# Performance work log

Measured on AMD Instinct MI355X. Metric: run time of the kernel, lower is better.

Reference implementation:

```python
import jax, jax.numpy as jnp
import numpy as np

N, F, H, C = 8192, 512, 512, 64
SPARSITY = 0.5  # args.linear_sparsity


def _percentile(t, q):
    # torch kthvalue semantics: k = 1 + round(0.01*q*(n-1)), 1-indexed k-th smallest
    n = t.size
    k = int(1 + round(0.01 * q * (n - 1)))
    return jnp.sort(t.ravel())[k - 1]


def _pair_norm(x):
    x = x - x.mean(axis=0)
    rownorm_mean = jnp.sqrt(1e-6 + (x * x).sum(axis=1).mean())
    return x / rownorm_mean


def setup_inputs() -> dict:
    key = jax.random.key(0)
    ks = jax.random.split(key, 8)
    x = jax.random.normal(ks[0], (N, F), jnp.float32)
    adj = (jax.random.uniform(ks[1], (N, N)) < 0.002).astype(jnp.float32)
    W0 = jax.random.normal(ks[2], (H, F), jnp.float32) * (1.0 / np.sqrt(F))
    W1 = jax.random.normal(ks[3], (H, H), jnp.float32) * (1.0 / np.sqrt(H))
    W2 = jax.random.normal(ks[4], (C, H), jnp.float32) * (1.0 / np.sqrt(H))
    S0 = jax.random.normal(ks[5], (H, F), jnp.float32)
    S1 = jax.random.normal(ks[6], (H, H), jnp.float32)
    S2 = jax.random.normal(ks[7], (C, H), jnp.float32)
    return {"x": x, "adj": adj, "W0": W0, "W1": W1, "W2": W2,
            "S0": S0, "S1": S1, "S2": S2}


def reference(x, adj, W0, W1, W2, S0, S1, S2):
    # add self loops
    idx = jnp.arange(N)
    adj = adj.at[idx, idx].set(1.0)
    # global threshold over all |score| params (enable_abs_comp=True)
    all_scores = jnp.concatenate([jnp.abs(S0).ravel(), jnp.abs(S1).ravel(), jnp.abs(S2).ravel()])
    thr = _percentile(all_scores, SPARSITY * 100.0)
    # symmetric normalization D^-1/2 A D^-1/2
    deg_inv_sqrt = jnp.maximum(adj.sum(axis=-1), 1.0) ** -0.5
    adj_n = deg_inv_sqrt[:, None] * adj * deg_inv_sqrt[None, :]

    def masked_linear(h, W, S):
        Wm = W * (jnp.abs(S) > thr).astype(W.dtype)
        return h @ Wm.T

    # layers 0..num_layers-2 applied back-to-back (as in the source loop)
    h = masked_linear(x, W0, S0)
    h = masked_linear(h, W1, S1)
    h = adj_n @ h            # aggregation: [N,N] @ [N,H]
    h = _pair_norm(h)
    h = jax.nn.relu(h)
    h = masked_linear(h, W2, S2)
    return adj_n @ h          # [N, C]
```

## Files before the change

kernel.cpp:

```cpp
#include <hip/hip_runtime.h>
#include <hip/hip_bf16.h>

#define NN 8192
#define FF 512
#define HH 512
#define CC 64
#define NS_TOTAL 557056
#define KSEL 278529u
#define MAXNBR 96
#define MASKB 2176

typedef short short8 __attribute__((ext_vector_type(8)));
typedef __bf16 bf16x8 __attribute__((ext_vector_type(8)));
typedef float f32x4 __attribute__((ext_vector_type(4)));

__device__ inline unsigned short f2bf(float f) {
    unsigned u = __float_as_uint(f);
    u += 0x7fffu + ((u >> 16) & 1u);
    return (unsigned short)(u >> 16);
}
__device__ inline float bf2f(unsigned short h) {
    return __uint_as_float(((unsigned)h) << 16);
}

__device__ inline f32x4 mfma16x16x32(short8 a, short8 b, f32x4 c) {
    return __builtin_amdgcn_mfma_f32_16x16x32_bf16(
        __builtin_bit_cast(bf16x8, a), __builtin_bit_cast(bf16x8, b), c, 0, 0, 0);
}

__device__ inline void gload_lds16(const unsigned short* g, unsigned short* l) {
    __builtin_amdgcn_global_load_lds(
        (const __attribute__((address_space(1))) void*)g,
        (__attribute__((address_space(3))) void*)l,
        16, 0, 0);
}

__device__ void deg_row_body(const float* __restrict__ adj, int* __restrict__ nnz,
                             int* __restrict__ colsI, float* __restrict__ dis,
                             int row, int* dcnt) {
    const int t = threadIdx.x;
    if (t == 0) *dcnt = 0;
    __syncthreads();
    const float4* arow = (const float4*)(adj + (size_t)row * NN);
    int* cp = colsI + (size_t)row * MAXNBR;
    for (int c4 = t; c4 < NN / 4; c4 += 256) {
        float4 v = arow[c4];
        int base = c4 * 4;
        float vv[4] = {v.x, v.y, v.z, v.w};
#pragma unroll
        for (int kq = 0; kq < 4; ++kq) {
            int col = base + kq;
            if (vv[kq] != 0.f || col == row) {
                int s = atomicAdd(dcnt, 1);
                if (s < MAXNBR) cp[s] = col;
            }
        }
    }
    __syncthreads();
    if (t == 0) {
        int c = *dcnt;
        nnz[row] = (c < MAXNBR) ? c : MAXNBR;
        dis[row] = rsqrtf((float)c);
    }
}

__device__ void isel(const unsigned* __restrict__ hist, unsigned k,
                     unsigned& bin, unsigned& krem) {
    __shared__ unsigned sh[256];
    __shared__ unsigned res[2];
    const int t = threadIdx.x;
    __syncthreads();
    sh[t] = hist[t];
    __syncthreads();
    unsigned pre = 0;
    for (int i = 0; i < t; ++i) pre += sh[i];
    if (pre < k && k <= pre + sh[t]) { res[0] = (unsigned)t; res[1] = k - pre; }
    __syncthreads();
    bin = res[0]; krem = res[1];
}

__device__ void isel_chain(const unsigned* __restrict__ hists, int npass,
                           unsigned& prefix, unsigned& k) {
    prefix = 0; k = KSEL;
    for (int p = 0; p < npass; ++p) {
        unsigned bin, krem;
        isel(hists + p * 256, k, bin, krem);
        prefix |= bin << (24 - 8 * p);
        k = krem;
    }
}


__global__ __launch_bounds__(256) void hist8_kernel(const float* __restrict__ S0,
                                                    const float* __restrict__ S1,
                                                    const float* __restrict__ S2,
                                                    unsigned* __restrict__ hists, int pass,
                                                    const float* __restrict__ adj,
                                                    int* __restrict__ nnz, int* __restrict__ colsI,
                                                    float* __restrict__ dis, int degRow0) {
    __shared__ unsigned lh[256];
    __shared__ int dcnt;
    if ((int)blockIdx.x >= 256) {
        deg_row_body(adj, nnz, colsI, dis, degRow0 + (int)blockIdx.x - 256, &dcnt);
        return;
    }
    unsigned prefix = 0, k;
    if (pass > 0) isel_chain(hists, pass, prefix, k);
    unsigned pmask = (pass > 0) ? (0xFFFFFFFFu << (32 - 8 * pass)) : 0u;
    int shift = 24 - 8 * pass;
    __syncthreads();
    lh[threadIdx.x] = 0;
    __syncthreads();
    for (int idx = blockIdx.x * 256 + threadIdx.x; idx < NS_TOTAL; idx += 65536) {
        float v = (idx < 262144) ? S0[idx] : (idx < 524288) ? S1[idx - 262144] : S2[idx - 524288];
        unsigned key = __float_as_uint(fabsf(v));
        if ((key & pmask) == prefix)
            atomicAdd(&lh[(key >> shift) & 0xffu], 1u);
    }
    __syncthreads();
    unsigned c = lh[threadIdx.x];
    if (c) atomicAdd(&hists[pass * 256 + threadIdx.x], c);
}


__global__ __launch_bounds__(256) void mask_split_fused(
        const float* __restrict__ W0, const float* __restrict__ W1,
        const float* __restrict__ W2, const float* __restrict__ S0,
        const float* __restrict__ S1, const float* __restrict__ S2,
        const unsigned* __restrict__ hists,
        unsigned short* __restrict__ W0h, unsigned short* __restrict__ W0l,
        unsigned short* __restrict__ W1h, unsigned short* __restrict__ W1l,
        unsigned short* __restrict__ W2h, unsigned short* __restrict__ W2l,
        const float* __restrict__ X,
        unsigned short* __restrict__ Xh, unsigned short* __restrict__ Xl) {
    if (blockIdx.x >= MASKB) {
        int i = (blockIdx.x - MASKB) * 256 + threadIdx.x;
        float4 v = ((const float4*)X)[i];
        float vv[4] = {v.x, v.y, v.z, v.w};
        ushort4 hi, lo;
        unsigned short* hp = (unsigned short*)&hi;
        unsigned short* lp = (unsigned short*)&lo;
#pragma unroll
        for (int j = 0; j < 4; ++j) {
            hp[j] = f2bf(vv[j]);
            lp[j] = f2bf(vv[j] - bf2f(hp[j]));
        }
        *(ushort4*)&Xh[(size_t)i * 4] = hi;
        *(ushort4*)&Xl[(size_t)i * 4] = lo;
        return;
    }
    unsigned prefix, k;
    isel_chain(hists, 4, prefix, k);
    float thr = __uint_as_float(prefix);
    int idx = blockIdx.x * 256 + threadIdx.x;
    const float* W; const float* S; unsigned short* Yh; unsigned short* Yl; int i;
    if (idx < 262144)      { W = W0; S = S0; Yh = W0h; Yl = W0l; i = idx; }
    else if (idx < 524288) { W = W1; S = S1; Yh = W1h; Yl = W1l; i = idx - 262144; }
    else                   { W = W2; S = S2; Yh = W2h; Yl = W2l; i = idx - 524288; }
    float v = (fabsf(S[i]) > thr) ? W[i] : 0.f;
    unsigned short hi = f2bf(v);
    Yh[i] = hi;
    Yl[i] = f2bf(v - bf2f(hi));
}


template<int BMt, int BNt, int WRITE_SPLIT>
__global__ __launch_bounds__(256) void gemm_hl(
        const unsigned short* __restrict__ Ah, const unsigned short* __restrict__ Al,
        const unsigned short* __restrict__ Bh, const unsigned short* __restrict__ Bl,
        float* __restrict__ Cf, unsigned short* __restrict__ Ch,
        unsigned short* __restrict__ Cl, int Nn, int gridN, int gemmBlocks,
        const float* __restrict__ adj, int* __restrict__ nnz, int* __restrict__ colsI,
        float* __restrict__ dis, int degRow0) {
    constexpr int BK = 32;
    constexpr int MF = BMt / 32, NF = BNt / 32;
    __shared__ __align__(16) unsigned short AhS[BMt * BK], AlS[BMt * BK];
    __shared__ __align__(16) unsigned short BhS[BNt * BK], BlS[BNt * BK];
    __shared__ int dcnt;

    if ((int)blockIdx.x >= gemmBlocks) {
        deg_row_body(adj, nnz, colsI, dis, degRow0 + (int)blockIdx.x - gemmBlocks, &dcnt);
        return;
    }
    const int tid = threadIdx.x, lane = tid & 63, wid = tid >> 6;
    const int wr = wid >> 1, wc = wid & 1;
    const int bm = ((int)blockIdx.x / gridN) * BMt;
    const int bn = ((int)blockIdx.x % gridN) * BNt;
    const int r16 = lane & 15, kg = lane >> 4;
    const int srow = lane >> 2;
    const int scol = ((lane & 3) ^ ((srow >> 1) & 3)) * 8;
    constexpr int cA = BMt / 16, cB = BNt / 16, CPW = (2 * cA + 2 * cB) / 4;
    f32x4 acc[MF][NF] = {};

    const int ksw = (kg ^ ((r16 >> 1) & 3)) * 8;
    const unsigned short* pAh = &AhS[(wr * (BMt / 2) + r16) * BK + ksw];
    const unsigned short* pAl = &AlS[(wr * (BMt / 2) + r16) * BK + ksw];
    const unsigned short* pBh = &BhS[(wc * (BNt / 2) + r16) * BK + ksw];
    const unsigned short* pBl = &BlS[(wc * (BNt / 2) + r16) * BK + ksw];

    for (int k0 = 0; k0 < 512; k0 += BK) {
        __syncthreads();
#pragma unroll
        for (int i = 0; i < CPW; ++i) {
            int c = wid * CPW + i;
            const unsigned short* src; unsigned short* dst; int cc, r0;
            if (c < cA)               { src = Ah; dst = AhS; cc = c;               r0 = bm + cc * 16; }
            else if (c < 2 * cA)      { src = Al; dst = AlS; cc = c - cA;          r0 = bm + cc * 16; }
            else if (c < 2 * cA + cB) { src = Bh; dst = BhS; cc = c - 2 * cA;      r0 = bn + cc * 16; }
            else                      { src = Bl; dst = BlS; cc = c - 2 * cA - cB; r0 = bn + cc * 16; }
            gload_lds16(src + (size_t)(r0 + srow) * 512 + k0 + scol, dst + cc * 512);
        }
        __syncthreads();
        short8 bhf[NF], blf[NF];
#pragma unroll
        for (int n = 0; n < NF; ++n) {
            bhf[n] = *(const short8*)(pBh + n * 16 * BK);
            blf[n] = *(const short8*)(pBl + n * 16 * BK);
        }
#pragma unroll
        for (int m = 0; m < MF; ++m) {
            short8 ahf = *(const short8*)(pAh + m * 16 * BK);
            short8 alf = *(const short8*)(pAl + m * 16 * BK);
#pragma unroll
            for (int n = 0; n < NF; ++n) {
                acc[m][n] = mfma16x16x32(ahf, bhf[n], acc[m][n]);
                acc[m][n] = mfma16x16x32(ahf, blf[n], acc[m][n]);
                acc[m][n] = mfma16x16x32(alf, bhf[n], acc[m][n]);
            }
        }
    }
#pragma unroll
    for (int m = 0; m < MF; ++m) {
#pragma unroll
        for (int n = 0; n < NF; ++n) {
            int row0 = bm + wr * (BMt / 2) + m * 16 + kg * 4;
            int col  = bn + wc * (BNt / 2) + n * 16 + r16;
#pragma unroll
            for (int j = 0; j < 4; ++j) {
                float v = acc[m][n][j];
                if (WRITE_SPLIT) {
                    unsigned short hi = f2bf(v);
                    size_t base = (size_t)(row0 + j) * Nn + col;
                    Ch[base] = hi;
                    Cl[base] = f2bf(v - bf2f(hi));
                } else {
                    Cf[(size_t)(row0 + j) * Nn + col] = v;
                }
            }
        }
    }
}


__global__ void spmm512(const int* __restrict__ nnz, const int* __restrict__ colsI,
                        const float* __restrict__ dis, const float* __restrict__ Hin,
                        float* __restrict__ Hout) {
    int row = blockIdx.x;
    int t = threadIdx.x;
    int cnt = nnz[row];
    const int* cp = colsI + (size_t)row * MAXNBR;
    float4 acc = make_float4(0.f, 0.f, 0.f, 0.f);
    for (int j = 0; j < cnt; ++j) {
        int c = cp[j];
        float wgt = dis[c];
        float4 v = *(const float4*)(Hin + (size_t)c * HH + t * 4);
        acc.x += wgt * v.x; acc.y += wgt * v.y; acc.z += wgt * v.z; acc.w += wgt * v.w;
    }
    float di = dis[row];
    acc.x *= di; acc.y *= di; acc.z *= di; acc.w *= di;
    *(float4*)(Hout + (size_t)row * HH + t * 4) = acc;
}

__global__ void spmm64(const int* __restrict__ nnz, const int* __restrict__ colsI,
                       const float* __restrict__ dis, const float* __restrict__ Hin,
                       float* __restrict__ Hout) {
    int row = blockIdx.x;
    int t = threadIdx.x;
    int cnt = nnz[row];
    const int* cp = colsI + (size_t)row * MAXNBR;
    float acc = 0.f;
    for (int j = 0; j < cnt; ++j) {
        int c = cp[j];
        acc += dis[c] * Hin[(size_t)c * CC + t];
    }
    Hout[(size_t)row * CC + t] = dis[row] * acc;
}


__global__ void colstats_kernel(const float* __restrict__ X, float* __restrict__ colsum,
                                float* __restrict__ stats) {
    int t = threadIdx.x;
    float s0 = 0.f, s1 = 0.f, sq = 0.f;
    for (int r = blockIdx.x; r < NN; r += 256) {
        const float* row = X + (size_t)r * HH;
        float a = row[t], b = row[t + 256];
        s0 += a; s1 += b;
        sq += a * a + b * b;
    }
    atomicAdd(&colsum[t], s0);
    atomicAdd(&colsum[t + 256], s1);
#pragma unroll
    for (int o = 32; o > 0; o >>= 1) sq += __shfl_down(sq, o);
    __shared__ float red[4];
    int wv = t >> 6, lane = t & 63;
    if (lane == 0) red[wv] = sq;
    __syncthreads();
    if (t == 0) atomicAdd(stats, red[0] + red[1] + red[2] + red[3]);
}

__global__ __launch_bounds__(256) void pn_apply_split(const float* __restrict__ X,
                                                      const float* __restrict__ colsum,
                                                      const float* __restrict__ stats,
                                                      unsigned short* __restrict__ Yh,
                                                      unsigned short* __restrict__ Yl) {
    const float inv = 1.0f / (float)NN;
    int t = threadIdx.x;
    float c0 = colsum[t], c1 = colsum[t + 256];
    float sq = c0 * c0 + c1 * c1;
#pragma unroll
    for (int o = 32; o > 0; o >>= 1) sq += __shfl_down(sq, o);
    __shared__ float red[4];
    __shared__ float sbc;
    int wv = t >> 6, lane = t & 63;
    if (lane == 0) red[wv] = sq;
    __syncthreads();
    if (t == 0) {
        float msum = red[0] + red[1] + red[2] + red[3];
        sbc = 1.0f / sqrtf(1e-6f + (stats[0] - msum * inv) * inv);
    }
    __syncthreads();
    float s = sbc;

    int i = blockIdx.x * 256 + t;
    float4 v = ((const float4*)X)[i];
    float4 m = ((const float4*)colsum)[i & 127];
    float vv[4];
    vv[0] = fmaxf((v.x - m.x * inv) * s, 0.f);
    vv[1] = fmaxf((v.y - m.y * inv) * s, 0.f);
    vv[2] = fmaxf((v.z - m.z * inv) * s, 0.f);
    vv[3] = fmaxf((v.w - m.w * inv) * s, 0.f);
    ushort4 hi, lo;
    unsigned short* hp = (unsigned short*)&hi;
    unsigned short* lp = (unsigned short*)&lo;
#pragma unroll
    for (int j = 0; j < 4; ++j) {
        hp[j] = f2bf(vv[j]);
        lp[j] = f2bf(vv[j] - bf2f(hp[j]));
    }
    *(ushort4*)&Yh[(size_t)i * 4] = hi;
    *(ushort4*)&Yl[(size_t)i * 4] = lo;
}


extern "C" void kernel_launch(void* const* d_in, const int* in_sizes, int n_in,
                              void* d_out, int out_size, void* d_ws, size_t ws_size,
                              hipStream_t stream) {
    const float* x   = (const float*)d_in[0];
    const float* adj = (const float*)d_in[1];
    const float* W0  = (const float*)d_in[2];
    const float* W1  = (const float*)d_in[3];
    const float* W2  = (const float*)d_in[4];
    const float* S0  = (const float*)d_in[5];
    const float* S1  = (const float*)d_in[6];
    const float* S2  = (const float*)d_in[7];
    float* out = (float*)d_out;

    char* w = (char*)d_ws;
    size_t off = 0;
    auto alloc = [&](size_t b) { size_t r = off; off = (off + b + 255) & ~(size_t)255; return r; };
    unsigned* hists = (unsigned*)(w + alloc(4 * 256 * 4));
    float* colsum   = (float*)(w + alloc(HH * 4));
    float* stats    = (float*)(w + alloc(256));
    size_t zero_end = off;
    int* nnz   = (int*)(w + alloc(NN * 4));
    int* colsI = (int*)(w + alloc((size_t)NN * MAXNBR * 4));
    float* dis = (float*)(w + alloc(NN * 4));
    unsigned short* xh  = (unsigned short*)(w + alloc((size_t)NN * FF * 2));
    unsigned short* xl  = (unsigned short*)(w + alloc((size_t)NN * FF * 2));
    unsigned short* W0h = (unsigned short*)(w + alloc((size_t)HH * FF * 2));
    unsigned short* W0l = (unsigned short*)(w + alloc((size_t)HH * FF * 2));
    unsigned short* W1h = (unsigned short*)(w + alloc((size_t)HH * HH * 2));
    unsigned short* W1l = (unsigned short*)(w + alloc((size_t)HH * HH * 2));
    unsigned short* W2h = (unsigned short*)(w + alloc((size_t)CC * HH * 2));
    unsigned short* W2l = (unsigned short*)(w + alloc((size_t)CC * HH * 2));
    unsigned short* hAh = (unsigned short*)(w + alloc((size_t)NN * HH * 2));
    unsigned short* hAl = (unsigned short*)(w + alloc((size_t)NN * HH * 2));
    float* hB   = (float*)(w + alloc((size_t)NN * HH * 4));
    float* hAgg = (float*)(w + alloc((size_t)NN * HH * 4));
    unsigned short* hBh = (unsigned short*)(w + alloc((size_t)NN * HH * 2));
    unsigned short* hBl = (unsigned short*)(w + alloc((size_t)NN * HH * 2));
    float* h3   = (float*)(w + alloc((size_t)NN * CC * 4));
    (void)ws_size; (void)in_sizes; (void)n_in; (void)out_size;

    hipMemsetAsync(d_ws, 0, zero_end, stream);

    for (int p = 0; p < 4; ++p)
        hist8_kernel<<<256 + 1024, 256, 0, stream>>>(S0, S1, S2, hists, p,
                                                     adj, nnz, colsI, dis, p * 1024);

    mask_split_fused<<<MASKB + NN * FF / 4 / 256, 256, 0, stream>>>(
        W0, W1, W2, S0, S1, S2, hists, W0h, W0l, W1h, W1l, W2h, W2l, x, xh, xl);

    const int g12 = (NN / 64) * (HH / 128);
    gemm_hl<64, 128, 1><<<g12 + 2048, 256, 0, stream>>>(
        xh, xl, W0h, W0l, nullptr, hAh, hAl, HH, HH / 128, g12,
        adj, nnz, colsI, dis, 4096);
    gemm_hl<64, 128, 0><<<g12 + 2048, 256, 0, stream>>>(
        hAh, hAl, W1h, W1l, hB, nullptr, nullptr, HH, HH / 128, g12,
        adj, nnz, colsI, dis, 6144);

    spmm512<<<NN, 128, 0, stream>>>(nnz, colsI, dis, hB, hAgg);

    colstats_kernel<<<256, 256, 0, stream>>>(hAgg, colsum, stats);
    pn_apply_split<<<(NN * HH / 4) / 256, 256, 0, stream>>>(hAgg, colsum, stats, hBh, hBl);

    const int g3 = (NN / 32) * (CC / 64);
    gemm_hl<32, 64, 0><<<g3, 256, 0, stream>>>(
        hBh, hBl, W2h, W2l, h3, nullptr, nullptr, CC, CC / 64, g3,
        nullptr, nullptr, nullptr, nullptr, 0);
    spmm64<<<NN, 64, 0, stream>>>(nnz, colsI, dis, h3, out);
}
```

Measured before the change: 226.9 us.

## Double-buffer GEMM LDS staging and move degree rows into histogram kernels

```diff
diff --git a/kernel.cpp b/kernel.cpp
--- a/kernel.cpp
+++ b/kernel.cpp
@@ -169,19 +169,12 @@
         const unsigned short* __restrict__ Ah, const unsigned short* __restrict__ Al,
         const unsigned short* __restrict__ Bh, const unsigned short* __restrict__ Bl,
         float* __restrict__ Cf, unsigned short* __restrict__ Ch,
-        unsigned short* __restrict__ Cl, int Nn, int gridN, int gemmBlocks,
-        const float* __restrict__ adj, int* __restrict__ nnz, int* __restrict__ colsI,
-        float* __restrict__ dis, int degRow0) {
+        unsigned short* __restrict__ Cl, int Nn, int gridN) {
     constexpr int BK = 32;
     constexpr int MF = BMt / 32, NF = BNt / 32;
-    __shared__ __align__(16) unsigned short AhS[BMt * BK], AlS[BMt * BK];
-    __shared__ __align__(16) unsigned short BhS[BNt * BK], BlS[BNt * BK];
-    __shared__ int dcnt;
-
-    if ((int)blockIdx.x >= gemmBlocks) {
-        deg_row_body(adj, nnz, colsI, dis, degRow0 + (int)blockIdx.x - gemmBlocks, &dcnt);
-        return;
-    }
+    __shared__ __align__(16) unsigned short AhS[2][BMt * BK], AlS[2][BMt * BK];
+    __shared__ __align__(16) unsigned short BhS[2][BNt * BK], BlS[2][BNt * BK];
+
     const int tid = threadIdx.x, lane = tid & 63, wid = tid >> 6;
     const int wr = wid >> 1, wc = wid & 1;
     const int bm = ((int)blockIdx.x / gridN) * BMt;
@@ -191,26 +184,25 @@
     const int scol = ((lane & 3) ^ ((srow >> 1) & 3)) * 8;
     constexpr int cA = BMt / 16, cB = BNt / 16, CPW = (2 * cA + 2 * cB) / 4;
     f32x4 acc[MF][NF] = {};
-
     const int ksw = (kg ^ ((r16 >> 1) & 3)) * 8;
-    const unsigned short* pAh = &AhS[(wr * (BMt / 2) + r16) * BK + ksw];
-    const unsigned short* pAl = &AlS[(wr * (BMt / 2) + r16) * BK + ksw];
-    const unsigned short* pBh = &BhS[(wc * (BNt / 2) + r16) * BK + ksw];
-    const unsigned short* pBl = &BlS[(wc * (BNt / 2) + r16) * BK + ksw];
-
-    for (int k0 = 0; k0 < 512; k0 += BK) {
-        __syncthreads();
+
+    auto STAGE = [&](int bf, int k0) {
 #pragma unroll
         for (int i = 0; i < CPW; ++i) {
             int c = wid * CPW + i;
             const unsigned short* src; unsigned short* dst; int cc, r0;
-            if (c < cA)               { src = Ah; dst = AhS; cc = c;               r0 = bm + cc * 16; }
-            else if (c < 2 * cA)      { src = Al; dst = AlS; cc = c - cA;          r0 = bm + cc * 16; }
-            else if (c < 2 * cA + cB) { src = Bh; dst = BhS; cc = c - 2 * cA;      r0 = bn + cc * 16; }
-            else                      { src = Bl; dst = BlS; cc = c - 2 * cA - cB; r0 = bn + cc * 16; }
+            if (c < cA)               { src = Ah; dst = AhS[bf]; cc = c;               r0 = bm + cc * 16; }
+            else if (c < 2 * cA)      { src = Al; dst = AlS[bf]; cc = c - cA;          r0 = bm + cc * 16; }
+            else if (c < 2 * cA + cB) { src = Bh; dst = BhS[bf]; cc = c - 2 * cA;      r0 = bn + cc * 16; }
+            else                      { src = Bl; dst = BlS[bf]; cc = c - 2 * cA - cB; r0 = bn + cc * 16; }
             gload_lds16(src + (size_t)(r0 + srow) * 512 + k0 + scol, dst + cc * 512);
         }
-        __syncthreads();
+    };
+    auto COMPUTE = [&](int bf) {
+        const unsigned short* pAh = &AhS[bf][(wr * (BMt / 2) + r16) * BK + ksw];
+        const unsigned short* pAl = &AlS[bf][(wr * (BMt / 2) + r16) * BK + ksw];
+        const unsigned short* pBh = &BhS[bf][(wc * (BNt / 2) + r16) * BK + ksw];
+        const unsigned short* pBl = &BlS[bf][(wc * (BNt / 2) + r16) * BK + ksw];
         short8 bhf[NF], blf[NF];
 #pragma unroll
         for (int n = 0; n < NF; ++n) {
@@ -228,6 +220,18 @@
                 acc[m][n] = mfma16x16x32(alf, bhf[n], acc[m][n]);
             }
         }
+    };
+
+    STAGE(0, 0);
+    __syncthreads();
+    for (int k0 = 0; k0 < 512; k0 += 64) {
+        STAGE(1, k0 + 32);
+        COMPUTE(0);
+        __syncthreads();
+        if (k0 + 64 < 512)
+            STAGE(0, k0 + 64);
+        COMPUTE(1);
+        __syncthreads();
     }
 #pragma unroll
     for (int m = 0; m < MF; ++m) {
@@ -395,28 +399,23 @@
     hipMemsetAsync(d_ws, 0, zero_end, stream);
 
     for (int p = 0; p < 4; ++p)
-        hist8_kernel<<<256 + 1024, 256, 0, stream>>>(S0, S1, S2, hists, p,
-                                                     adj, nnz, colsI, dis, p * 1024);
+        hist8_kernel<<<256 + 2048, 256, 0, stream>>>(S0, S1, S2, hists, p,
+                                                     adj, nnz, colsI, dis, p * 2048);
 
     mask_split_fused<<<MASKB + NN * FF / 4 / 256, 256, 0, stream>>>(
         W0, W1, W2, S0, S1, S2, hists, W0h, W0l, W1h, W1l, W2h, W2l, x, xh, xl);
 
-    const int g12 = (NN / 64) * (HH / 128);
-    gemm_hl<64, 128, 1><<<g12 + 2048, 256, 0, stream>>>(
-        xh, xl, W0h, W0l, nullptr, hAh, hAl, HH, HH / 128, g12,
-        adj, nnz, colsI, dis, 4096);
-    gemm_hl<64, 128, 0><<<g12 + 2048, 256, 0, stream>>>(
-        hAh, hAl, W1h, W1l, hB, nullptr, nullptr, HH, HH / 128, g12,
-        adj, nnz, colsI, dis, 6144);
+    gemm_hl<64, 128, 1><<<(NN / 64) * (HH / 128), 256, 0, stream>>>(
+        xh, xl, W0h, W0l, nullptr, hAh, hAl, HH, HH / 128);
+    gemm_hl<64, 128, 0><<<(NN / 64) * (HH / 128), 256, 0, stream>>>(
+        hAh, hAl, W1h, W1l, hB, nullptr, nullptr, HH, HH / 128);
 
     spmm512<<<NN, 128, 0, stream>>>(nnz, colsI, dis, hB, hAgg);
 
     colstats_kernel<<<256, 256, 0, stream>>>(hAgg, colsum, stats);
     pn_apply_split<<<(NN * HH / 4) / 256, 256, 0, stream>>>(hAgg, colsum, stats, hBh, hBl);
 
-    const int g3 = (NN / 32) * (CC / 64);
-    gemm_hl<32, 64, 0><<<g3, 256, 0, stream>>>(
-        hBh, hBl, W2h, W2l, h3, nullptr, nullptr, CC, CC / 64, g3,
-        nullptr, nullptr, nullptr, nullptr, 0);
+    gemm_hl<32, 64, 0><<<(NN / 32) * (CC / 64), 256, 0, stream>>>(
+        hBh, hBl, W2h, W2l, h3, nullptr, nullptr, CC, CC / 64);
     spmm64<<<NN, 64, 0, stream>>>(nnz, colsI, dis, h3, out);
 }
```

Result: no change. 226.1 us (-0.4%).

## Fuse PairNorm column statistics into GEMM and SpMM epilogues, drop colstats kernel

Applied to the files above, without the earlier changes.

```diff
diff --git a/kernel.cpp b/kernel.cpp
--- a/kernel.cpp
+++ b/kernel.cpp
@@ -37,7 +37,7 @@
 
 __device__ void deg_row_body(const float* __restrict__ adj, int* __restrict__ nnz,
                              int* __restrict__ colsI, float* __restrict__ dis,
-                             int row, int* dcnt) {
+                             float* __restrict__ uvec, int row, int* dcnt, float* dshare) {
     const int t = threadIdx.x;
     if (t == 0) *dcnt = 0;
     __syncthreads();
@@ -59,9 +59,17 @@
     __syncthreads();
     if (t == 0) {
         int c = *dcnt;
-        nnz[row] = (c < MAXNBR) ? c : MAXNBR;
-        dis[row] = rsqrtf((float)c);
-    }
+        int cl = (c < MAXNBR) ? c : MAXNBR;
+        nnz[row] = cl;
+        float d = rsqrtf((float)c);
+        dis[row] = d;
+        *dshare = d;
+        *dcnt = cl;
+    }
+    __syncthreads();
+    float dr = *dshare;
+    int cl = *dcnt;
+    if (t < cl) atomicAdd(&uvec[cp[t]], dr);
 }
 
 __device__ void isel(const unsigned* __restrict__ hist, unsigned k,
@@ -97,11 +105,14 @@
                                                     unsigned* __restrict__ hists, int pass,
                                                     const float* __restrict__ adj,
                                                     int* __restrict__ nnz, int* __restrict__ colsI,
-                                                    float* __restrict__ dis, int degRow0) {
+                                                    float* __restrict__ dis,
+                                                    float* __restrict__ uvec, int degRow0) {
     __shared__ unsigned lh[256];
     __shared__ int dcnt;
+    __shared__ float dshare;
     if ((int)blockIdx.x >= 256) {
-        deg_row_body(adj, nnz, colsI, dis, degRow0 + (int)blockIdx.x - 256, &dcnt);
+        deg_row_body(adj, nnz, colsI, dis, uvec, degRow0 + (int)blockIdx.x - 256,
+                     &dcnt, &dshare);
         return;
     }
     unsigned prefix = 0, k;
@@ -164,24 +175,20 @@
 }
 
 
-template<int BMt, int BNt, int WRITE_SPLIT>
+template<int BMt, int BNt, int WRITE_SPLIT, int COLSUM>
 __global__ __launch_bounds__(256) void gemm_hl(
         const unsigned short* __restrict__ Ah, const unsigned short* __restrict__ Al,
         const unsigned short* __restrict__ Bh, const unsigned short* __restrict__ Bl,
         float* __restrict__ Cf, unsigned short* __restrict__ Ch,
-        unsigned short* __restrict__ Cl, int Nn, int gridN, int gemmBlocks,
-        const float* __restrict__ adj, int* __restrict__ nnz, int* __restrict__ colsI,
-        float* __restrict__ dis, int degRow0) {
+        unsigned short* __restrict__ Cl, int Nn, int gridN,
+        const float* __restrict__ dis, const float* __restrict__ uvec,
+        float* __restrict__ colsum) {
     constexpr int BK = 32;
     constexpr int MF = BMt / 32, NF = BNt / 32;
     __shared__ __align__(16) unsigned short AhS[BMt * BK], AlS[BMt * BK];
     __shared__ __align__(16) unsigned short BhS[BNt * BK], BlS[BNt * BK];
-    __shared__ int dcnt;
-
-    if ((int)blockIdx.x >= gemmBlocks) {
-        deg_row_body(adj, nnz, colsI, dis, degRow0 + (int)blockIdx.x - gemmBlocks, &dcnt);
-        return;
-    }
+    __shared__ float csPart[COLSUM ? BNt : 1];
+
     const int tid = threadIdx.x, lane = tid & 63, wid = tid >> 6;
     const int wr = wid >> 1, wc = wid & 1;
     const int bm = ((int)blockIdx.x / gridN) * BMt;
@@ -191,13 +198,15 @@
     const int scol = ((lane & 3) ^ ((srow >> 1) & 3)) * 8;
     constexpr int cA = BMt / 16, cB = BNt / 16, CPW = (2 * cA + 2 * cB) / 4;
     f32x4 acc[MF][NF] = {};
-
     const int ksw = (kg ^ ((r16 >> 1) & 3)) * 8;
     const unsigned short* pAh = &AhS[(wr * (BMt / 2) + r16) * BK + ksw];
     const unsigned short* pAl = &AlS[(wr * (BMt / 2) + r16) * BK + ksw];
     const unsigned short* pBh = &BhS[(wc * (BNt / 2) + r16) * BK + ksw];
     const unsigned short* pBl = &BlS[(wc * (BNt / 2) + r16) * BK + ksw];
 
+    if (COLSUM) {
+        for (int i = tid; i < BNt; i += 256) csPart[i] = 0.f;
+    }
     for (int k0 = 0; k0 < 512; k0 += BK) {
         __syncthreads();
 #pragma unroll
@@ -245,16 +254,24 @@
                     Cl[base] = f2bf(v - bf2f(hi));
                 } else {
                     Cf[(size_t)(row0 + j) * Nn + col] = v;
+                    if (COLSUM) {
+                        float wrow = dis[row0 + j] * uvec[row0 + j];
+                        atomicAdd(&csPart[col - bn], wrow * v);
+                    }
                 }
             }
         }
     }
+    if (COLSUM) {
+        __syncthreads();
+        for (int i = tid; i < BNt; i += 256) atomicAdd(&colsum[bn + i], csPart[i]);
+    }
 }
 
 
 __global__ void spmm512(const int* __restrict__ nnz, const int* __restrict__ colsI,
                         const float* __restrict__ dis, const float* __restrict__ Hin,
-                        float* __restrict__ Hout) {
+                        float* __restrict__ Hout, float* __restrict__ stats) {
     int row = blockIdx.x;
     int t = threadIdx.x;
     int cnt = nnz[row];
@@ -269,6 +286,13 @@
     float di = dis[row];
     acc.x *= di; acc.y *= di; acc.z *= di; acc.w *= di;
     *(float4*)(Hout + (size_t)row * HH + t * 4) = acc;
+    float sq = acc.x * acc.x + acc.y * acc.y + acc.z * acc.z + acc.w * acc.w;
+#pragma unroll
+    for (int o = 32; o > 0; o >>= 1) sq += __shfl_down(sq, o);
+    __shared__ float red[2];
+    if ((t & 63) == 0) red[t >> 6] = sq;
+    __syncthreads();
+    if (t == 0) atomicAdd(stats, red[0] + red[1]);
 }
 
 __global__ void spmm64(const int* __restrict__ nnz, const int* __restrict__ colsI,
@@ -284,28 +308,6 @@
         acc += dis[c] * Hin[(size_t)c * CC + t];
     }
     Hout[(size_t)row * CC + t] = dis[row] * acc;
-}
-
-
-__global__ void colstats_kernel(const float* __restrict__ X, float* __restrict__ colsum,
-                                float* __restrict__ stats) {
-    int t = threadIdx.x;
-    float s0 = 0.f, s1 = 0.f, sq = 0.f;
-    for (int r = blockIdx.x; r < NN; r += 256) {
-        const float* row = X + (size_t)r * HH;
-        float a = row[t], b = row[t + 256];
-        s0 += a; s1 += b;
-        sq += a * a + b * b;
-    }
-    atomicAdd(&colsum[t], s0);
-    atomicAdd(&colsum[t + 256], s1);
-#pragma unroll
-    for (int o = 32; o > 0; o >>= 1) sq += __shfl_down(sq, o);
-    __shared__ float red[4];
-    int wv = t >> 6, lane = t & 63;
-    if (lane == 0) red[wv] = sq;
-    __syncthreads();
-    if (t == 0) atomicAdd(stats, red[0] + red[1] + red[2] + red[3]);
 }
 
 __global__ __launch_bounds__(256) void pn_apply_split(const float* __restrict__ X,
@@ -371,6 +373,7 @@
     unsigned* hists = (unsigned*)(w + alloc(4 * 256 * 4));
     float* colsum   = (float*)(w + alloc(HH * 4));
     float* stats    = (float*)(w + alloc(256));
+    float* uvec     = (float*)(w + alloc(NN * 4));
     size_t zero_end = off;
     int* nnz   = (int*)(w + alloc(NN * 4));
     int* colsI = (int*)(w + alloc((size_t)NN * MAXNBR * 4));
@@ -395,28 +398,22 @@
     hipMemsetAsync(d_ws, 0, zero_end, stream);
 
     for (int p = 0; p < 4; ++p)
-        hist8_kernel<<<256 + 1024, 256, 0, stream>>>(S0, S1, S2, hists, p,
-                                                     adj, nnz, colsI, dis, p * 1024);
+        hist8_kernel<<<256 + 2048, 256, 0, stream>>>(S0, S1, S2, hists, p,
+                                                     adj, nnz, colsI, dis, uvec, p * 2048);
 
     mask_split_fused<<<MASKB + NN * FF / 4 / 256, 256, 0, stream>>>(
         W0, W1, W2, S0, S1, S2, hists, W0h, W0l, W1h, W1l, W2h, W2l, x, xh, xl);
 
-    const int g12 = (NN / 64) * (HH / 128);
-    gemm_hl<64, 128, 1><<<g12 + 2048, 256, 0, stream>>>(
-        xh, xl, W0h, W0l, nullptr, hAh, hAl, HH, HH / 128, g12,
-        adj, nnz, colsI, dis, 4096);
-    gemm_hl<64, 128, 0><<<g12 + 2048, 256, 0, stream>>>(
-        hAh, hAl, W1h, W1l, hB, nullptr, nullptr, HH, HH / 128, g12,
-        adj, nnz, colsI, dis, 6144);
-
-    spmm512<<<NN, 128, 0, stream>>>(nnz, colsI, dis, hB, hAgg);
-
-    colstats_kernel<<<256, 256, 0, stream>>>(hAgg, colsum, stats);
+    gemm_hl<64, 128, 1, 0><<<(NN / 64) * (HH / 128), 256, 0, stream>>>(
+        xh, xl, W0h, W0l, nullptr, hAh, hAl, HH, HH / 128, nullptr, nullptr, nullptr);
+    gemm_hl<64, 128, 0, 1><<<(NN / 64) * (HH / 128), 256, 0, stream>>>(
+        hAh, hAl, W1h, W1l, hB, nullptr, nullptr, HH, HH / 128, dis, uvec, colsum);
+
+    spmm512<<<NN, 128, 0, stream>>>(nnz, colsI, dis, hB, hAgg, stats);
+
     pn_apply_split<<<(NN * HH / 4) / 256, 256, 0, stream>>>(hAgg, colsum, stats, hBh, hBl);
 
-    const int g3 = (NN / 32) * (CC / 64);
-    gemm_hl<32, 64, 0><<<g3, 256, 0, stream>>>(
-        hBh, hBl, W2h, W2l, h3, nullptr, nullptr, CC, CC / 64, g3,
-        nullptr, nullptr, nullptr, nullptr, 0);
+    gemm_hl<32, 64, 0, 0><<<(NN / 32) * (CC / 64), 256, 0, stream>>>(
+        hBh, hBl, W2h, W2l, h3, nullptr, nullptr, CC, CC / 64, nullptr, nullptr, nullptr);
     spmm64<<<NN, 64, 0, stream>>>(nnz, colsI, dis, h3, out);
 }
```

Result: slower. 323.0 us (+42.4%).

## Fuse pair-norm apply into final GEMM and move degree work into histogram kernel

Applied to the files above, without the earlier changes.

```diff
diff --git a/kernel.cpp b/kernel.cpp
--- a/kernel.cpp
+++ b/kernel.cpp
@@ -169,19 +169,12 @@
         const unsigned short* __restrict__ Ah, const unsigned short* __restrict__ Al,
         const unsigned short* __restrict__ Bh, const unsigned short* __restrict__ Bl,
         float* __restrict__ Cf, unsigned short* __restrict__ Ch,
-        unsigned short* __restrict__ Cl, int Nn, int gridN, int gemmBlocks,
-        const float* __restrict__ adj, int* __restrict__ nnz, int* __restrict__ colsI,
-        float* __restrict__ dis, int degRow0) {
+        unsigned short* __restrict__ Cl, int Nn, int gridN) {
     constexpr int BK = 32;
     constexpr int MF = BMt / 32, NF = BNt / 32;
     __shared__ __align__(16) unsigned short AhS[BMt * BK], AlS[BMt * BK];
     __shared__ __align__(16) unsigned short BhS[BNt * BK], BlS[BNt * BK];
-    __shared__ int dcnt;
-
-    if ((int)blockIdx.x >= gemmBlocks) {
-        deg_row_body(adj, nnz, colsI, dis, degRow0 + (int)blockIdx.x - gemmBlocks, &dcnt);
-        return;
-    }
+
     const int tid = threadIdx.x, lane = tid & 63, wid = tid >> 6;
     const int wr = wid >> 1, wc = wid & 1;
     const int bm = ((int)blockIdx.x / gridN) * BMt;
@@ -191,7 +184,6 @@
     const int scol = ((lane & 3) ^ ((srow >> 1) & 3)) * 8;
     constexpr int cA = BMt / 16, cB = BNt / 16, CPW = (2 * cA + 2 * cB) / 4;
     f32x4 acc[MF][NF] = {};
-
     const int ksw = (kg ^ ((r16 >> 1) & 3)) * 8;
     const unsigned short* pAh = &AhS[(wr * (BMt / 2) + r16) * BK + ksw];
     const unsigned short* pAl = &AlS[(wr * (BMt / 2) + r16) * BK + ksw];
@@ -248,6 +240,107 @@
                 }
             }
         }
+    }
+}
+
+
+__global__ __launch_bounds__(256) void gemm3_pn(
+        const float* __restrict__ hAgg,
+        const unsigned short* __restrict__ Bh, const unsigned short* __restrict__ Bl,
+        const float* __restrict__ colsum, const float* __restrict__ stats,
+        float* __restrict__ Cf) {
+    constexpr int BMt = 32, BNt = 64, BK = 32;
+    constexpr int NF = 2;
+    __shared__ __align__(16) unsigned short AhS[BMt * BK], AlS[BMt * BK];
+    __shared__ __align__(16) unsigned short BhS[BNt * BK], BlS[BNt * BK];
+    __shared__ float red[4];
+    __shared__ float sbc;
+
+    const int tid = threadIdx.x, lane = tid & 63, wid = tid >> 6;
+    const int wr = wid >> 1, wc = wid & 1;
+    const int bm = (int)blockIdx.x * BMt;
+    const int r16 = lane & 15, kg = lane >> 4;
+    const int srow = lane >> 2;
+    const int scol = ((lane & 3) ^ ((srow >> 1) & 3)) * 8;
+    const float inv = 1.0f / (float)NN;
+
+    {
+        float c0 = colsum[tid], c1 = colsum[tid + 256];
+        float sq = c0 * c0 + c1 * c1;
+#pragma unroll
+        for (int o = 32; o > 0; o >>= 1) sq += __shfl_down(sq, o);
+        if ((tid & 63) == 0) red[tid >> 6] = sq;
+        __syncthreads();
+        if (tid == 0) {
+            float msum = red[0] + red[1] + red[2] + red[3];
+            sbc = 1.0f / sqrtf(1e-6f + (stats[0] - msum * inv) * inv);
+        }
+        __syncthreads();
+    }
+    const float s = sbc;
+
+    const int ar = tid >> 3, ac = (tid & 7) * 4;
+    const int aoff = ar * 64 + (((ac >> 3) ^ ((ar >> 1) & 3)) * 16) + (ac & 7) * 2;
+
+    f32x4 acc[1][NF] = {};
+    const int ksw = (kg ^ ((r16 >> 1) & 3)) * 8;
+    const unsigned short* pAh = &AhS[(wr * 16 + r16) * BK + ksw];
+    const unsigned short* pAl = &AlS[(wr * 16 + r16) * BK + ksw];
+    const unsigned short* pBh = &BhS[(wc * 32 + r16) * BK + ksw];
+    const unsigned short* pBl = &BlS[(wc * 32 + r16) * BK + ksw];
+
+    for (int k0 = 0; k0 < 512; k0 += BK) {
+        __syncthreads();
+#pragma unroll
+        for (int i = 0; i < 2; ++i) {
+            int c = wid * 2 + i;
+            const unsigned short* src = (c < 4) ? Bh : Bl;
+            unsigned short* dst = (c < 4) ? BhS : BlS;
+            int cc = c & 3;
+            gload_lds16(src + (size_t)(cc * 16 + srow) * 512 + k0 + scol, dst + cc * 512);
+        }
+        {
+            float4 av = *(const float4*)(hAgg + (size_t)(bm + ar) * HH + k0 + ac);
+            float4 m4 = *(const float4*)(colsum + k0 + ac);
+            float vv[4];
+            vv[0] = fmaxf((av.x - m4.x * inv) * s, 0.f);
+            vv[1] = fmaxf((av.y - m4.y * inv) * s, 0.f);
+            vv[2] = fmaxf((av.z - m4.z * inv) * s, 0.f);
+            vv[3] = fmaxf((av.w - m4.w * inv) * s, 0.f);
+            ushort4 hi, lo;
+            unsigned short* hp = (unsigned short*)&hi;
+            unsigned short* lp = (unsigned short*)&lo;
+#pragma unroll
+            for (int j = 0; j < 4; ++j) {
+                hp[j] = f2bf(vv[j]);
+                lp[j] = f2bf(vv[j] - bf2f(hp[j]));
+            }
+            *(ushort4*)((char*)AhS + aoff) = hi;
+            *(ushort4*)((char*)AlS + aoff) = lo;
+        }
+        __syncthreads();
+        short8 bhf[NF], blf[NF];
+#pragma unroll
+        for (int n = 0; n < NF; ++n) {
+            bhf[n] = *(const short8*)(pBh + n * 16 * BK);
+            blf[n] = *(const short8*)(pBl + n * 16 * BK);
+        }
+        short8 ahf = *(const short8*)pAh;
+        short8 alf = *(const short8*)pAl;
+#pragma unroll
+        for (int n = 0; n < NF; ++n) {
+            acc[0][n] = mfma16x16x32(ahf, bhf[n], acc[0][n]);
+            acc[0][n] = mfma16x16x32(ahf, blf[n], acc[0][n]);
+            acc[0][n] = mfma16x16x32(alf, bhf[n], acc[0][n]);
+        }
+    }
+#pragma unroll
+    for (int n = 0; n < NF; ++n) {
+        int row0 = bm + wr * 16 + kg * 4;
+        int col  = wc * 32 + n * 16 + r16;
+#pragma unroll
+        for (int j = 0; j < 4; ++j)
+            Cf[(size_t)(row0 + j) * CC + col] = acc[0][n][j];
     }
 }
 
@@ -306,49 +399,6 @@
     if (lane == 0) red[wv] = sq;
     __syncthreads();
     if (t == 0) atomicAdd(stats, red[0] + red[1] + red[2] + red[3]);
-}
-
-__global__ __launch_bounds__(256) void pn_apply_split(const float* __restrict__ X,
-                                                      const float* __restrict__ colsum,
-                                                      const float* __restrict__ stats,
-                                                      unsigned short* __restrict__ Yh,
-                                                      unsigned short* __restrict__ Yl) {
-    const float inv = 1.0f / (float)NN;
-    int t = threadIdx.x;
-    float c0 = colsum[t], c1 = colsum[t + 256];
-    float sq = c0 * c0 + c1 * c1;
-#pragma unroll
-    for (int o = 32; o > 0; o >>= 1) sq += __shfl_down(sq, o);
-    __shared__ float red[4];
-    __shared__ float sbc;
-    int wv = t >> 6, lane = t & 63;
-    if (lane == 0) red[wv] = sq;
-    __syncthreads();
-    if (t == 0) {
-        float msum = red[0] + red[1] + red[2] + red[3];
-        sbc = 1.0f / sqrtf(1e-6f + (stats[0] - msum * inv) * inv);
-    }
-    __syncthreads();
-    float s = sbc;
-
-    int i = blockIdx.x * 256 + t;
-    float4 v = ((const float4*)X)[i];
-    float4 m = ((const float4*)colsum)[i & 127];
-    float vv[4];
-    vv[0] = fmaxf((v.x - m.x * inv) * s, 0.f);
-    vv[1] = fmaxf((v.y - m.y * inv) * s, 0.f);
-    vv[2] = fmaxf((v.z - m.z * inv) * s, 0.f);
-    vv[3] = fmaxf((v.w - m.w * inv) * s, 0.f);
-    ushort4 hi, lo;
-    unsigned short* hp = (unsigned short*)&hi;
-    unsigned short* lp = (unsigned short*)&lo;
-#pragma unroll
-    for (int j = 0; j < 4; ++j) {
-        hp[j] = f2bf(vv[j]);
-        lp[j] = f2bf(vv[j] - bf2f(hp[j]));
-    }
-    *(ushort4*)&Yh[(size_t)i * 4] = hi;
-    *(ushort4*)&Yl[(size_t)i * 4] = lo;
 }
 
 
@@ -387,36 +437,27 @@
     unsigned short* hAl = (unsigned short*)(w + alloc((size_t)NN * HH * 2));
     float* hB   = (float*)(w + alloc((size_t)NN * HH * 4));
     float* hAgg = (float*)(w + alloc((size_t)NN * HH * 4));
-    unsigned short* hBh = (unsigned short*)(w + alloc((size_t)NN * HH * 2));
-    unsigned short* hBl = (unsigned short*)(w + alloc((size_t)NN * HH * 2));
     float* h3   = (float*)(w + alloc((size_t)NN * CC * 4));
     (void)ws_size; (void)in_sizes; (void)n_in; (void)out_size;
 
     hipMemsetAsync(d_ws, 0, zero_end, stream);
 
     for (int p = 0; p < 4; ++p)
-        hist8_kernel<<<256 + 1024, 256, 0, stream>>>(S0, S1, S2, hists, p,
-                                                     adj, nnz, colsI, dis, p * 1024);
+        hist8_kernel<<<256 + 2048, 256, 0, stream>>>(S0, S1, S2, hists, p,
+                                                     adj, nnz, colsI, dis, p * 2048);
 
     mask_split_fused<<<MASKB + NN * FF / 4 / 256, 256, 0, stream>>>(
         W0, W1, W2, S0, S1, S2, hists, W0h, W0l, W1h, W1l, W2h, W2l, x, xh, xl);
 
-    const int g12 = (NN / 64) * (HH / 128);
-    gemm_hl<64, 128, 1><<<g12 + 2048, 256, 0, stream>>>(
-        xh, xl, W0h, W0l, nullptr, hAh, hAl, HH, HH / 128, g12,
-        adj, nnz, colsI, dis, 4096);
-    gemm_hl<64, 128, 0><<<g12 + 2048, 256, 0, stream>>>(
-        hAh, hAl, W1h, W1l, hB, nullptr, nullptr, HH, HH / 128, g12,
-        adj, nnz, colsI, dis, 6144);
+    gemm_hl<64, 128, 1><<<(NN / 64) * (HH / 128), 256, 0, stream>>>(
+        xh, xl, W0h, W0l, nullptr, hAh, hAl, HH, HH / 128);
+    gemm_hl<64, 128, 0><<<(NN / 64) * (HH / 128), 256, 0, stream>>>(
+        hAh, hAl, W1h, W1l, hB, nullptr, nullptr, HH, HH / 128);
 
     spmm512<<<NN, 128, 0, stream>>>(nnz, colsI, dis, hB, hAgg);
 
     colstats_kernel<<<256, 256, 0, stream>>>(hAgg, colsum, stats);
-    pn_apply_split<<<(NN * HH / 4) / 256, 256, 0, stream>>>(hAgg, colsum, stats, hBh, hBl);
-
-    const int g3 = (NN / 32) * (CC / 64);
-    gemm_hl<32, 64, 0><<<g3, 256, 0, stream>>>(
-        hBh, hBl, W2h, W2l, h3, nullptr, nullptr, CC, CC / 64, g3,
-        nullptr, nullptr, nullptr, nullptr, 0);
+
+    gemm3_pn<<<NN / 32, 256, 0, stream>>>(hAgg, W2h, W2l, colsum, stats, h3);
     spmm64<<<NN, 64, 0, stream>>>(nnz, colsI, dis, h3, out);
 }
```

After: 224.9 us. About the same (-0.9%).
